# Optimization experiments

Measured on AMD Instinct MI355X. Metric: run time of the kernel, lower is better.

The kernel has to match this reference:

```python
import jax, jax.numpy as jnp
import numpy as np

N_NODES = 100000
N_EDGES = 1600000
IN_CH = 64
HID = 64
OUT_CH = 32


def _init_lin(key, fan_in, fan_out):
    # uniform(-1/sqrt(fan_in), 1/sqrt(fan_in)) like torch Linear
    b = 1.0 / np.sqrt(fan_in)
    return jax.random.uniform(key, (fan_in, fan_out), jnp.float32, -b, b)


def setup_inputs() -> dict:
    key = jax.random.key(0)
    ks = jax.random.split(key, 16)
    x = jax.random.normal(ks[0], (N_NODES, IN_CH), jnp.float32)
    edge_index = jax.random.randint(ks[1], (2, N_EDGES), 0, N_NODES, jnp.int64)
    params = {}
    dims = [(IN_CH, HID), (HID, HID), (HID, HID)]
    for i, (fi, fo) in enumerate(dims, start=1):
        params[f"Wl{i}"] = _init_lin(ks[3 * i], fi, fo)       # applied to aggregated neighbors
        params[f"Wr{i}"] = _init_lin(ks[3 * i + 1], fi, fo)   # applied to root features
        params[f"b{i}"] = jnp.zeros((fo,), jnp.float32)
    params["Wlin"] = _init_lin(ks[12], HID, OUT_CH)
    params["blin"] = jnp.zeros((OUT_CH,), jnp.float32)
    return {"x": x, "edge_index": edge_index, **params}


def _mean_aggregate(x, src, dst, n_nodes):
    # mean of source-node features over incoming edges per destination node
    msg_sum = jax.ops.segment_sum(x[src], dst, num_segments=n_nodes)
    deg = jax.ops.segment_sum(jnp.ones((src.shape[0], 1), x.dtype), dst, num_segments=n_nodes)
    return msg_sum / jnp.maximum(deg, 1.0)


def _sage_conv(x, src, dst, Wl, Wr, b):
    # PyG SAGEConv (mean aggr): out = lin_l(mean_j x_j) + lin_r(x_i)
    agg = _mean_aggregate(x, src, dst, x.shape[0])
    return agg @ Wl + b + x @ Wr


def reference(x, edge_index, Wl1, Wr1, b1, Wl2, Wr2, b2, Wl3, Wr3, b3, Wlin, blin):
    src, dst = edge_index[0], edge_index[1]
    h = jax.nn.relu(_sage_conv(x, src, dst, Wl1, Wr1, b1))
    h = jax.nn.relu(_sage_conv(h, src, dst, Wl2, Wr2, b2))
    h = jax.nn.relu(_sage_conv(h, src, dst, Wl3, Wr3, b3))
    return h @ Wlin + blin
```

## Files before the change

kernel.cpp:

```cpp
#include <hip/hip_runtime.h>
#include <hip/hip_bf16.h>

#define N_NODES 100000
#define N_EDGES 1600000
#define HID 64
#define OUT_CH 32

#define NB 196
#define P 1024
#define EPP ((N_EDGES + P - 1) / P)
#define BKCAP 10240
#define MP 72

typedef unsigned short ushort_t;
typedef short bf16x8 __attribute__((ext_vector_type(8)));
typedef float f32x4 __attribute__((ext_vector_type(4)));

__device__ __forceinline__ ushort_t f2b(float f) {
    union { float f; unsigned u; } un; un.f = f;
    unsigned r = un.u + 0x7FFF + ((un.u >> 16) & 1);
    return (ushort_t)(r >> 16);
}
__device__ __forceinline__ float blo(unsigned u) {
    union { unsigned u; float f; } un; un.u = u << 16; return un.f;
}
__device__ __forceinline__ float bhi(unsigned u) {
    union { unsigned u; float f; } un; un.u = u & 0xFFFF0000u; return un.f;
}

__device__ __forceinline__ int get_dst(const int* __restrict__ ei, int is64, int e) {
    return is64 ? ((const int2*)ei)[N_EDGES + e].x : ei[N_EDGES + e];
}
__device__ __forceinline__ int get_src(const int* __restrict__ ei, int is64, int e) {
    return is64 ? ((const int2*)ei)[e].x : ei[e];
}

__device__ __forceinline__ void detect_is64(const int* __restrict__ ei,
                                            int* __restrict__ sflag, int tid) {
    if (tid < 64) {
        int v = ei[2 * tid + 1];
        unsigned long long ball = __ballot(v == 0);
        if (tid == 0) *sflag = (ball == ~0ull) ? 1 : 0;
    }
}

#define CONV_BLOCKS ((N_NODES * HID / 4) / 256)
__global__ void __launch_bounds__(256) convhist_kernel(
        const float* __restrict__ x, ushort_t* __restrict__ xb,
        const int* __restrict__ ei, int* __restrict__ histG,
        const float* __restrict__ W0, const float* __restrict__ W1,
        const float* __restrict__ W2, const float* __restrict__ W3,
        const float* __restrict__ W4, const float* __restrict__ W5,
        ushort_t* __restrict__ wpk) {
    int bid = blockIdx.x;
    if (bid >= CONV_BLOCKS) {
        const float* Ws[6] = {W0, W1, W2, W3, W4, W5};
        int w = bid - CONV_BLOCKS;
        const float* W = Ws[w];
        ushort_t* d = wpk + w * 4096;
        for (int idx = threadIdx.x; idx < 4096; idx += 256) {
            int j = idx & 7;
            int ln = (idx >> 3) & 63;
            int t = idx >> 9;
            int ks = t & 1, nt = t >> 1;
            int k = ks * 32 + (ln >> 4) * 8 + j;
            int n = nt * 16 + (ln & 15);
            d[idx] = f2b(W[k * HID + n]);
        }
        return;
    }
    int i = bid * 256 + threadIdx.x;
    if (i < N_NODES * HID / 4) {
        float4 v = ((const float4*)x)[i];
        ushort4 o;
        o.x = f2b(v.x); o.y = f2b(v.y); o.z = f2b(v.z); o.w = f2b(v.w);
        ((ushort4*)xb)[i] = o;
    }
    if (bid >= P) return;
    __shared__ int sflag;
    __shared__ int lh[NB];
    int tid = threadIdx.x;
    detect_is64(ei, &sflag, tid);
    for (int k = tid; k < NB; k += 256) lh[k] = 0;
    __syncthreads();
    int is64 = sflag;
    int e0 = bid * EPP;
    int e1 = min(e0 + EPP, N_EDGES);
    for (int e = e0 + tid; e < e1; e += 256) {
        int d = get_dst(ei, is64, e);
        atomicAdd(&lh[d >> 9], 1);
    }
    __syncthreads();
    for (int k = tid; k < NB; k += 256) histG[k * P + bid] = lh[k];
}

__global__ void __launch_bounds__(256) scan_kernel(int* __restrict__ histG,
                                                   int* __restrict__ btot) {
    __shared__ int ps[256];
    int b = blockIdx.x;
    int tid = threadIdx.x;
    int base4 = b * P + 4 * tid;
    int v0 = histG[base4], v1 = histG[base4 + 1], v2 = histG[base4 + 2], v3 = histG[base4 + 3];
    int pv = v0 + v1 + v2 + v3;
    ps[tid] = pv;
    __syncthreads();
    for (int d = 1; d < 256; d <<= 1) {
        int t = (tid >= d) ? ps[tid - d] : 0;
        __syncthreads();
        ps[tid] += t;
        __syncthreads();
    }
    int e = ps[tid] - pv;
    histG[base4] = e; e += v0;
    histG[base4 + 1] = e; e += v1;
    histG[base4 + 2] = e; e += v2;
    histG[base4 + 3] = e;
    if (tid == 255) btot[b] = ps[255];
}

__global__ void __launch_bounds__(256) place_kernel(
        const int* __restrict__ ei, const int* __restrict__ histG,
        const int* __restrict__ btot, int* __restrict__ bkt) {
    __shared__ int lcur[NB];
    __shared__ int ss[256];
    __shared__ int sflag;
    int tid = threadIdx.x;
    detect_is64(ei, &sflag, tid);
    int v = (tid < NB) ? btot[tid] : 0;
    ss[tid] = v;
    __syncthreads();
    for (int d = 1; d < 256; d <<= 1) {
        int t = (tid >= d) ? ss[tid - d] : 0;
        __syncthreads();
        ss[tid] += t;
        __syncthreads();
    }
    if (tid < NB) lcur[tid] = (ss[tid] - v) + histG[tid * P + blockIdx.x];
    __syncthreads();
    int is64 = sflag;
    int e0 = blockIdx.x * EPP;
    int e1 = min(e0 + EPP, N_EDGES);
    for (int e = e0 + tid; e < e1; e += 256) {
        int s = get_src(ei, is64, e);
        int d = get_dst(ei, is64, e);
        int val = ((d & 511) << 17) | s;
        int p = atomicAdd(&lcur[d >> 9], 1);
        bkt[p] = val;
    }
}

__global__ void __launch_bounds__(256) bucket_fill_kernel(
        const int* __restrict__ btot, const int* __restrict__ bkt,
        int* __restrict__ csr, unsigned int* __restrict__ offpk) {
    __shared__ int lcnt[512];
    __shared__ int loff[512];
    __shared__ int lcur[512];
    __shared__ int ps[256];
    __shared__ int scsr[BKCAP];
    __shared__ int sbase;
    int b = blockIdx.x;
    int tid = threadIdx.x;
    int m = btot[b];
    int vb = (tid < NB) ? btot[tid] : 0;
    ps[tid] = vb;
    __syncthreads();
    for (int d = 1; d < 256; d <<= 1) {
        int t = (tid >= d) ? ps[tid - d] : 0;
        __syncthreads();
        ps[tid] += t;
        __syncthreads();
    }
    if (tid == b) sbase = ps[tid] - vb;
    __syncthreads();
    int base = sbase;
    int n0 = b << 9;
    int nn = min(512, N_NODES - n0);

    lcnt[tid] = 0;
    lcnt[tid + 256] = 0;
    __syncthreads();
    for (int i = tid; i < m; i += 256) atomicAdd(&lcnt[bkt[base + i] >> 17], 1);
    __syncthreads();
    int a0 = lcnt[2 * tid], a1 = lcnt[2 * tid + 1];
    int pv = a0 + a1;
    ps[tid] = pv;
    __syncthreads();
    for (int d = 1; d < 256; d <<= 1) {
        int t = (tid >= d) ? ps[tid - d] : 0;
        __syncthreads();
        ps[tid] += t;
        __syncthreads();
    }
    int excl = ps[tid] - pv;
    loff[2 * tid] = excl;
    loff[2 * tid + 1] = excl + a0;
    lcur[2 * tid] = excl;
    lcur[2 * tid + 1] = excl + a0;
    __syncthreads();
    bool fit = (m <= BKCAP);
    for (int i = tid; i < m; i += 256) {
        int val = bkt[base + i];
        int dl = val >> 17;
        int p = atomicAdd(&lcur[dl], 1);
        if (fit) scsr[p] = val & 0x1FFFF;
        else csr[base + p] = val & 0x1FFFF;
    }
    __syncthreads();
    if (fit)
        for (int i = tid; i < m; i += 256) csr[base + i] = scsr[i];
    for (int i = tid; i < nn; i += 256)
        offpk[n0 + i] = (unsigned int)((base + loff[i]) | (lcnt[i] << 21));
}

template <bool FUSE_HEAD>
__global__ void __launch_bounds__(512, 4) fused_gather_layer(
        const ushort_t* __restrict__ featin,
        const unsigned int* __restrict__ offpk, const int* __restrict__ csr,
        const ushort_t* __restrict__ wpk, const float* __restrict__ bias,
        ushort_t* __restrict__ featout,
        const float* __restrict__ Wlin, const float* __restrict__ blin,
        float* __restrict__ out) {
    __shared__ __align__(16) ushort_t sWlF[4096];
    __shared__ __align__(16) ushort_t sWrF[4096];
    __shared__ __align__(16) ushort_t sA[64 * MP];
    __shared__ __align__(16) ushort_t sH[64 * MP];
    __shared__ float sbias[HID];
    __shared__ float sWo[FUSE_HEAD ? HID * OUT_CH : 1];
    __shared__ float sbo[FUSE_HEAD ? OUT_CH : 1];
    int tid = threadIdx.x;
    int node0 = blockIdx.x * 64;

    ((int4*)sWlF)[tid] = ((const int4*)wpk)[tid];
    ((int4*)sWrF)[tid] = ((const int4*)wpk)[512 + tid];
    if (tid < HID) sbias[tid] = bias[tid];
    if constexpr (FUSE_HEAD) {
        ((int4*)sWo)[tid] = ((const int4*)Wlin)[tid];
        if (tid < OUT_CH) sbo[tid] = blin[tid];
    }
    {
        const int4* gh = (const int4*)(featin + (size_t)node0 * HID);
        int r = tid >> 3, u = tid & 7;
        *(int4*)(sH + r * MP + u * 8) = gh[tid];
    }

    int wv = tid >> 6, ln = tid & 63;
    int g = ln >> 3;
    int l = ln & 7;
    int nl = wv * 8 + g;
    int node = node0 + nl;
    unsigned int v = (node < N_NODES) ? offpk[node] : 0u;
    int off = (int)(v & 0x1FFFFFu);
    int cnt = (int)(v >> 21);
    float a0 = 0.f, a1 = 0.f, a2 = 0.f, a3 = 0.f;
    float a4 = 0.f, a5 = 0.f, a6 = 0.f, a7 = 0.f;
    int gbase = g << 3;
    for (int b = 0; b < cnt; b += 16) {
        int rem = cnt - b;
        int e0 = (l < rem) ? csr[off + b + l] : 0;
        int e1 = (l + 8 < rem) ? csr[off + b + 8 + l] : 0;
        int4 u[16];
#pragma unroll
        for (int j = 0; j < 8; ++j)
            u[j] = ((const int4*)(featin + (size_t)__shfl(e0, gbase + j) * HID))[l];
#pragma unroll
        for (int j = 0; j < 8; ++j)
            u[8 + j] = ((const int4*)(featin + (size_t)__shfl(e1, gbase + j) * HID))[l];
#pragma unroll
        for (int j = 0; j < 16; ++j) {
            if (j >= rem) { u[j].x = 0; u[j].y = 0; u[j].z = 0; u[j].w = 0; }
            a0 += blo(u[j].x); a1 += bhi(u[j].x);
            a2 += blo(u[j].y); a3 += bhi(u[j].y);
            a4 += blo(u[j].z); a5 += bhi(u[j].z);
            a6 += blo(u[j].w); a7 += bhi(u[j].w);
        }
    }
    {
        float inv = 1.f / fmaxf((float)cnt, 1.f);
        int4 w;
        w.x = (int)((unsigned)f2b(a0 * inv) | ((unsigned)f2b(a1 * inv) << 16));
        w.y = (int)((unsigned)f2b(a2 * inv) | ((unsigned)f2b(a3 * inv) << 16));
        w.z = (int)((unsigned)f2b(a4 * inv) | ((unsigned)f2b(a5 * inv) << 16));
        w.w = (int)((unsigned)f2b(a6 * inv) | ((unsigned)f2b(a7 * inv) << 16));
        *(int4*)(sA + nl * MP + l * 8) = w;
    }
    __syncthreads();

    int lane = ln;
    int quad = lane >> 4, col = lane & 15;
    int mt = wv >> 1, npb = (wv & 1) * 2;
    int arow = mt * 16 + col;
    bf16x8 aA0 = *(const bf16x8*)(sA + arow * MP + quad * 8);
    bf16x8 aA1 = *(const bf16x8*)(sA + arow * MP + 32 + quad * 8);
    bf16x8 aH0 = *(const bf16x8*)(sH + arow * MP + quad * 8);
    bf16x8 aH1 = *(const bf16x8*)(sH + arow * MP + 32 + quad * 8);
    ushort_t hv[2][4];
#pragma unroll
    for (int t = 0; t < 2; ++t) {
        int nt = npb + t;
        f32x4 acc = {0.f, 0.f, 0.f, 0.f};
        const bf16x8* bl = (const bf16x8*)(sWlF + nt * 1024);
        const bf16x8* br = (const bf16x8*)(sWrF + nt * 1024);
        acc = __builtin_amdgcn_mfma_f32_16x16x32_bf16(aA0, bl[lane], acc, 0, 0, 0);
        acc = __builtin_amdgcn_mfma_f32_16x16x32_bf16(aA1, bl[64 + lane], acc, 0, 0, 0);
        acc = __builtin_amdgcn_mfma_f32_16x16x32_bf16(aH0, br[lane], acc, 0, 0, 0);
        acc = __builtin_amdgcn_mfma_f32_16x16x32_bf16(aH1, br[64 + lane], acc, 0, 0, 0);
        float bv = sbias[nt * 16 + col];
#pragma unroll
        for (int r = 0; r < 4; ++r) {
            ushort_t hb16 = f2b(fmaxf(acc[r] + bv, 0.f));
            if constexpr (FUSE_HEAD) {
                hv[t][r] = hb16;
            } else {
                int n = node0 + mt * 16 + quad * 4 + r;
                if (n < N_NODES)
                    featout[(size_t)n * HID + nt * 16 + col] = hb16;
            }
        }
    }

    if constexpr (FUSE_HEAD) {
        __syncthreads();
#pragma unroll
        for (int t = 0; t < 2; ++t)
#pragma unroll
            for (int r = 0; r < 4; ++r)
                sA[(mt * 16 + quad * 4 + r) * MP + (npb + t) * 16 + col] = hv[t][r];
        __syncthreads();

        int c0 = (tid & 7) << 2;
        int n0 = tid >> 3;
        float acc2[4];
#pragma unroll
        for (int j = 0; j < 4; ++j) acc2[j] = sbo[c0 + j];
#pragma unroll 4
        for (int kk = 0; kk < 32; ++kk) {
            float4 w0 = *(const float4*)&sWo[(2 * kk) * OUT_CH + c0];
            float4 w1 = *(const float4*)&sWo[(2 * kk + 1) * OUT_CH + c0];
            const float* w0p = (const float*)&w0;
            const float* w1p = (const float*)&w1;
            unsigned uh = *(const unsigned*)(sA + n0 * MP + 2 * kk);
            float h0 = blo(uh), h1 = bhi(uh);
#pragma unroll
            for (int j = 0; j < 4; ++j) acc2[j] += h0 * w0p[j] + h1 * w1p[j];
        }
        int n = node0 + n0;
        if (n < N_NODES) {
            float4 o4;
            o4.x = acc2[0]; o4.y = acc2[1]; o4.z = acc2[2]; o4.w = acc2[3];
            *(float4*)(out + (size_t)n * OUT_CH + c0) = o4;
        }
    }
}

extern "C" void kernel_launch(void* const* d_in, const int* in_sizes, int n_in,
                              void* d_out, int out_size, void* d_ws, size_t ws_size,
                              hipStream_t stream) {
    const float* x    = (const float*)d_in[0];
    const int*   ei   = (const int*)d_in[1];
    const float* Wl1  = (const float*)d_in[2];
    const float* Wr1  = (const float*)d_in[3];
    const float* b1   = (const float*)d_in[4];
    const float* Wl2  = (const float*)d_in[5];
    const float* Wr2  = (const float*)d_in[6];
    const float* b2   = (const float*)d_in[7];
    const float* Wl3  = (const float*)d_in[8];
    const float* Wr3  = (const float*)d_in[9];
    const float* b3   = (const float*)d_in[10];
    const float* Wlin = (const float*)d_in[11];
    const float* blin = (const float*)d_in[12];
    float* out = (float*)d_out;

    int* ip              = (int*)d_ws;
    unsigned int* offpk  = (unsigned int*)ip;
    int* btot            = (int*)(offpk + 100096);
    int* histG           = btot + 256;
    int* csr             = histG + NB * P;
    int* bkt             = csr + N_EDGES;
    ushort_t* featbA     = (ushort_t*)(bkt + N_EDGES);
    ushort_t* featbB     = featbA + 6408192;
    ushort_t* wpk        = featbB + 6408192;

    const int TILE_BLOCKS = (N_NODES + 63) / 64;

    convhist_kernel<<<CONV_BLOCKS + 6, 256, 0, stream>>>(
        x, featbA, ei, histG, Wl1, Wr1, Wl2, Wr2, Wl3, Wr3, wpk);
    scan_kernel<<<NB, 256, 0, stream>>>(histG, btot);
    place_kernel<<<P, 256, 0, stream>>>(ei, histG, btot, bkt);
    bucket_fill_kernel<<<NB, 256, 0, stream>>>(btot, bkt, csr, offpk);

    fused_gather_layer<false><<<TILE_BLOCKS, 512, 0, stream>>>(
        featbA, offpk, csr, wpk, b1, featbB, nullptr, nullptr, nullptr);

    fused_gather_layer<false><<<TILE_BLOCKS, 512, 0, stream>>>(
        featbB, offpk, csr, wpk + 8192, b2, featbA, nullptr, nullptr, nullptr);

    fused_gather_layer<true><<<TILE_BLOCKS, 512, 0, stream>>>(
        featbA, offpk, csr, wpk + 16384, b3, nullptr, Wlin, blin, out);
}
```

Measured before the change: 245.9 us.

## Locally sort edges by bucket in LDS before writing bucket array

The place kernel now stages each block's edges in shared memory, counts them per bucket, prefix-sums the counts, and scatters them into a locally bucket-sorted LDS buffer. It then writes them to global memory in sorted order, so consecutive threads write contiguous runs within each bucket. This is meant to replace scattered global writes with more coalesced ones. The cost is extra LDS traffic, another scan with its barriers, and more shared memory per block, which may lower occupancy.

```diff
diff --git a/kernel.cpp b/kernel.cpp
--- a/kernel.cpp
+++ b/kernel.cpp
@@ -121,9 +121,17 @@
 __global__ void __launch_bounds__(256) place_kernel(
         const int* __restrict__ ei, const int* __restrict__ histG,
         const int* __restrict__ btot, int* __restrict__ bkt) {
-    __shared__ int lcur[NB];
     __shared__ int ss[256];
     __shared__ int sflag;
+    __shared__ int gb0[NB];
+    __shared__ int lcnt[NB];
+    __shared__ int lrun[256];
+    __shared__ int gbase[NB];
+    __shared__ int lcur[NB];
+    __shared__ int valbuf[EPP];
+    __shared__ unsigned char kbuf[EPP];
+    __shared__ int sortv[EPP];
+    __shared__ int sorta[EPP];
     int tid = threadIdx.x;
     detect_is64(ei, &sflag, tid);
     int v = (tid < NB) ? btot[tid] : 0;
@@ -135,18 +143,47 @@
         ss[tid] += t;
         __syncthreads();
     }
-    if (tid < NB) lcur[tid] = (ss[tid] - v) + histG[tid * P + blockIdx.x];
+    if (tid < NB) gb0[tid] = (ss[tid] - v) + histG[tid * P + blockIdx.x];
+    for (int k = tid; k < NB; k += 256) lcnt[k] = 0;
     __syncthreads();
     int is64 = sflag;
     int e0 = blockIdx.x * EPP;
     int e1 = min(e0 + EPP, N_EDGES);
-    for (int e = e0 + tid; e < e1; e += 256) {
+    int m = e1 - e0;
+    for (int i = tid; i < m; i += 256) {
+        int e = e0 + i;
         int s = get_src(ei, is64, e);
         int d = get_dst(ei, is64, e);
-        int val = ((d & 511) << 17) | s;
-        int p = atomicAdd(&lcur[d >> 9], 1);
-        bkt[p] = val;
-    }
+        valbuf[i] = ((d & 511) << 17) | s;
+        int k = d >> 9;
+        kbuf[i] = (unsigned char)k;
+        atomicAdd(&lcnt[k], 1);
+    }
+    __syncthreads();
+    int c = (tid < NB) ? lcnt[tid] : 0;
+    lrun[tid] = c;
+    __syncthreads();
+    for (int d = 1; d < 256; d <<= 1) {
+        int t = (tid >= d) ? lrun[tid - d] : 0;
+        __syncthreads();
+        lrun[tid] += t;
+        __syncthreads();
+    }
+    if (tid < NB) {
+        int excl = lrun[tid] - c;
+        gbase[tid] = gb0[tid] - excl;
+        lcur[tid] = excl;
+    }
+    __syncthreads();
+    for (int i = tid; i < m; i += 256) {
+        int k = kbuf[i];
+        int p = atomicAdd(&lcur[k], 1);
+        sortv[p] = valbuf[i];
+        sorta[p] = gbase[k];
+    }
+    __syncthreads();
+    for (int i = tid; i < m; i += 256)
+        bkt[sorta[i] + i] = sortv[i];
 }
 
 __global__ void __launch_bounds__(256) bucket_fill_kernel(
```

Result: faster. 240.9 us, median of 2 (-2.0%).
